# Kernel tuning notes

Measured on AMD Instinct MI355X. Metric: run time of the kernel, lower is better.

## Reference

```python
import jax, jax.numpy as jnp
import numpy as np

EPS = 1e-5  # torch LayerNorm default


def _ln(x, w, b):
    m = jnp.mean(x, axis=-1, keepdims=True)
    v = jnp.mean((x - m) ** 2, axis=-1, keepdims=True)
    return (x - m) / jnp.sqrt(v + EPS) * w + b


def _conv1x1(x, w, b):
    # x: [B,C,H,W], w: [O,C], b: [O]
    return jnp.einsum('bchw,oc->bohw', x, w) + b[None, :, None, None]


def setup_inputs() -> dict:
    key = jax.random.key(0)
    ks = jax.random.split(key, 5)
    B, Cin, H, W = 8, 384, 64, 64
    D, N = 128, 512
    s = lambda k, shape, scale=0.02: jax.random.normal(k, shape, jnp.float32) * scale
    return {
        'x': jax.random.normal(ks[0], (B, Cin, H, W), jnp.float32),
        'DR': jax.random.normal(ks[1], (N, D), jnp.float32),
        'conv_in_w': s(ks[2], (D, Cin)),
        'conv_in_b': jnp.zeros((D,), jnp.float32),
        'sem_w': s(ks[3], (D, D)),
        'sem_b': jnp.zeros((D,), jnp.float32),
        'norm1_w': jnp.ones((D,), jnp.float32),
        'norm1_b': jnp.zeros((D,), jnp.float32),
        'norm2_w': jnp.ones((D,), jnp.float32),
        'norm2_b': jnp.zeros((D,), jnp.float32),
        'conv_out_w': s(ks[4], (Cin, D)),
        'conv_out_b': jnp.zeros((Cin,), jnp.float32),
    }


def reference(x, DR, conv_in_w, conv_in_b, sem_w, sem_b, norm1_w, norm1_b,
              norm2_w, norm2_b, conv_out_w, conv_out_b):
    B, _, H, W = x.shape
    N = DR.shape[0]
    x_align = _conv1x1(x, conv_in_w, conv_in_b)                      # [B,D,H,W]
    x_sem = _conv1x1(x_align, sem_w, sem_b)                          # semantic_extra (1x1 conv)
    x_sem = x_sem.transpose(0, 2, 3, 1).reshape(B, H * W, -1)        # [B,HW,D]
    x_sem = _ln(x_sem, norm1_w, norm1_b)
    dr = _ln(DR, norm2_w, norm2_b).T                                 # [D,N] (same for all batches)
    # NOTE: original applies norm_1 TWICE for the numerator (faithful quirk)
    c_u = jnp.einsum('bld,dn->bln', _ln(x_sem, norm1_w, norm1_b), dr)  # [B,HW,N]
    c_d_l = jnp.sqrt(jnp.sum(x_sem ** 2, axis=-1, keepdims=True))      # [B,HW,1]
    c_d_r = jnp.sqrt(jnp.sum(dr ** 2, axis=0, keepdims=True))[None]    # [1,1,N]
    sim = c_u / (c_d_l * c_d_r)
    sim_soft = jax.nn.softmax(sim, axis=-1)                          # [B,HW,N]
    sim2d = sim_soft.transpose(0, 2, 1).reshape(B, N, H, W)
    degrad = jnp.einsum('bln,dn->bdl', sim_soft, dr).reshape(B, -1, H, W)  # [B,D,H,W]
    # pow-mask with per-batch min-max normalization
    mask_v = jnp.max(sim2d ** 3, axis=1, keepdims=True)              # [B,1,H,W]
    mn = jnp.min(mask_v.reshape(B, -1), axis=1).reshape(B, 1, 1, 1)
    mx = jnp.max(mask_v.reshape(B, -1), axis=1).reshape(B, 1, 1, 1)
    mask_v = 1.0 - (mask_v - mn) / (mx - mn)
    # topk row selection (torch fancy indexing gives [B,B,K,N]; squeeze(1) is a no-op for B>1)
    max_values = jnp.max(sim_soft, axis=2)                           # [B,HW]
    K = (H * W) // 50
    _, top_idx = jax.lax.top_k(max_values, K)                        # [B,K]
    results = jnp.take(sim_soft, top_idx, axis=1)                    # [B,B,K,N]
    out_img = _conv1x1(degrad, conv_out_w, conv_out_b)               # [B,Cin,H,W]
    return (mask_v, out_img, results)
```

## Files before the change

kernel.cpp:

```cpp
#include <hip/hip_runtime.h>
#include <cstdint>

#define EPS 1e-5f
#define BB   8
#define CIN  384
#define HWs  4096
#define LT   32768
#define DD   128
#define NN   512
#define TOPK 81
#define PSTR 528

typedef short short8 __attribute__((ext_vector_type(8)));
typedef float f32x4  __attribute__((ext_vector_type(4)));

__device__ __forceinline__ unsigned short f2bf(float x) {
  unsigned u = __float_as_uint(x);
  u += 0x7fffu + ((u >> 16) & 1u);
  return (unsigned short)(u >> 16);
}
__device__ __forceinline__ float bf2f(unsigned u16) {
  return __uint_as_float(u16 << 16);
}
__device__ __forceinline__ void put_frag(unsigned short* buf, int tile, int rc, int k, float v) {
  int ks = k >> 5, g = (k >> 3) & 3, j = k & 7;
  int basehw = ((tile * 4 + ks) * 2) * 512 + (g * 16 + rc) * 8 + j;
  unsigned short hi = f2bf(v);
  buf[basehw] = hi;
  buf[basehw + 512] = f2bf(v - bf2f(hi));
}

__global__ __launch_bounds__(64) void k_dr(const float* __restrict__ DR,
    const float* __restrict__ w2, const float* __restrict__ b2,
    const float* __restrict__ w1, const float* __restrict__ b1,
    unsigned short* __restrict__ drwF, unsigned short* __restrict__ drlnF,
    float* __restrict__ t2, float* __restrict__ rcr) {
  int n = blockIdx.x;
  int lane = threadIdx.x;
  const float* row = DR + n * DD;
  float x0 = row[lane], x1 = row[lane + 64];
  float s = x0 + x1, sq = x0 * x0 + x1 * x1;
  #pragma unroll
  for (int o = 32; o; o >>= 1) { s += __shfl_xor(s, o); sq += __shfl_xor(sq, o); }
  float m = s * (1.f / 128.f);
  float v = sq * (1.f / 128.f) - m * m;
  float inv = rsqrtf(v + EPS);
  float y0 = (x0 - m) * inv * w2[lane] + b2[lane];
  float y1 = (x1 - m) * inv * w2[lane + 64] + b2[lane + 64];
  int nt = n >> 4, cc = n & 15;
  put_frag(drwF, nt, cc, lane, y0 * w1[lane]);
  put_frag(drwF, nt, cc, lane + 64, y1 * w1[lane + 64]);
  int ks = n >> 5, gB = (n >> 3) & 3, j = n & 7;
  {
    int d = lane;
    unsigned short hi = f2bf(y0);
    int base = (((d >> 4) * 16 + ks) * 2) * 512 + (gB * 16 + (d & 15)) * 8 + j;
    drlnF[base] = hi;
    drlnF[base + 512] = f2bf(y0 - bf2f(hi));
  }
  {
    int d = lane + 64;
    unsigned short hi = f2bf(y1);
    int base = (((d >> 4) * 16 + ks) * 2) * 512 + (gB * 16 + (d & 15)) * 8 + j;
    drlnF[base] = hi;
    drlnF[base + 512] = f2bf(y1 - bf2f(hi));
  }
  float pt2 = y0 * b1[lane] + y1 * b1[lane + 64];
  float pss = y0 * y0 + y1 * y1;
  #pragma unroll
  for (int o = 32; o; o >>= 1) { pt2 += __shfl_xor(pt2, o); pss += __shfl_xor(pss, o); }
  if (lane == 0) { t2[n] = pt2; rcr[n] = rsqrtf(pss); }
}

__global__ __launch_bounds__(256) void k_bprep(const float* __restrict__ src,
                                               unsigned short* __restrict__ dst,
                                               int K) {
  int rt = blockIdx.x, kb = blockIdx.y;
  int t = threadIdx.x, m = t >> 4, kg = t & 15;
  int k0 = kb * 128 + kg * 8;
  const float* s = src + (size_t)(rt * 16 + m) * K + k0;
  float4 f0 = *(const float4*)s;
  float4 f1 = *(const float4*)(s + 4);
  float vs[8] = {f0.x, f0.y, f0.z, f0.w, f1.x, f1.y, f1.z, f1.w};
  short8 hi, lo;
  #pragma unroll
  for (int j = 0; j < 8; ++j) {
    unsigned short h = f2bf(vs[j]);
    hi[j] = (short)h;
    lo[j] = (short)f2bf(vs[j] - bf2f(h));
  }
  int nkt = K >> 5;
  int ks = k0 >> 5, g = (k0 >> 3) & 3;
  short8* D8 = (short8*)dst;
  int base = ((rt * nkt + ks) * 2) * 64 + g * 16 + m;
  D8[base] = hi;
  D8[base + 64] = lo;
}

__global__ __launch_bounds__(256, 3) void k_convsem(const float* __restrict__ x,
    const unsigned short* __restrict__ WinF, const float* __restrict__ bin,
    const unsigned short* __restrict__ semWF, const float* __restrict__ sb,
    const float* __restrict__ w1, const float* __restrict__ b1,
    unsigned short* __restrict__ ApF, float* __restrict__ rclv) {
  __shared__ float xt[CIN * 33];
  __shared__ float sredS[32][4], sredQ[32][4];
  __shared__ float rowM[32], rowI[32];
  int t = threadIdx.x;
  int w = t >> 6, lane = t & 63, m = lane & 15, g = lane >> 4;
  int l0 = blockIdx.x * 32;
  int b = l0 >> 12, hw0 = l0 & 4095;
  {
    const float* xs = x + (size_t)b * CIN * HWs + (size_t)(t >> 3) * HWs + hw0 + (t & 7) * 4;
    float4 v[12];
    #pragma unroll
    for (int r = 0; r < 12; ++r)
      v[r] = *(const float4*)(xs + (size_t)(r * 32) * HWs);
    #pragma unroll
    for (int r = 0; r < 12; ++r) {
      float* d = &xt[(r * 32 + (t >> 3)) * 33 + (t & 7) * 4];
      d[0] = v[r].x; d[1] = v[r].y; d[2] = v[r].z; d[3] = v[r].w;
    }
  }
  __syncthreads();
  const short8* B8 = (const short8*)WinF;
  f32x4 acc[2][2];
  #pragma unroll
  for (int lt = 0; lt < 2; ++lt)
    #pragma unroll
    for (int j2 = 0; j2 < 2; ++j2) acc[lt][j2] = (f32x4){0.f, 0.f, 0.f, 0.f};
  for (int ks = 0; ks < 12; ++ks) {
    short8 ah[2], al[2];
    #pragma unroll
    for (int lt = 0; lt < 2; ++lt) {
      #pragma unroll
      for (int j = 0; j < 8; ++j) {
        float xv = xt[(ks * 32 + g * 8 + j) * 33 + lt * 16 + m];
        unsigned short h = f2bf(xv);
        ah[lt][j] = (short)h;
        al[lt][j] = (short)f2bf(xv - bf2f(h));
      }
    }
    #pragma unroll
    for (int j2 = 0; j2 < 2; ++j2) {
      int dt = w * 2 + j2;
      short8 bh = B8[((dt * 12 + ks) * 2 + 0) * 64 + lane];
      short8 bl = B8[((dt * 12 + ks) * 2 + 1) * 64 + lane];
      #pragma unroll
      for (int lt = 0; lt < 2; ++lt) {
        acc[lt][j2] = __builtin_amdgcn_mfma_f32_16x16x32_bf16(ah[lt], bh, acc[lt][j2], 0, 0, 0);
        acc[lt][j2] = __builtin_amdgcn_mfma_f32_16x16x32_bf16(ah[lt], bl, acc[lt][j2], 0, 0, 0);
        acc[lt][j2] = __builtin_amdgcn_mfma_f32_16x16x32_bf16(al[lt], bh, acc[lt][j2], 0, 0, 0);
      }
    }
  }
  __syncthreads();
  unsigned int* plane = (unsigned int*)xt;
  {
    float bia[2] = {bin[w * 32 + m], bin[w * 32 + 16 + m]};
    #pragma unroll
    for (int lt = 0; lt < 2; ++lt)
      #pragma unroll
      for (int j2 = 0; j2 < 2; ++j2)
        #pragma unroll
        for (int r = 0; r < 4; ++r) {
          float v = acc[lt][j2][r] + bia[j2];
          unsigned short h = f2bf(v);
          unsigned short lo = f2bf(v - bf2f(h));
          plane[(lt * 16 + g * 4 + r) * 132 + (w * 2 + j2) * 16 + m] =
              (unsigned)h | ((unsigned)lo << 16);
        }
  }
  __syncthreads();
  const short8* S8 = (const short8*)semWF;
  f32x4 acc2[2][2];
  #pragma unroll
  for (int lt = 0; lt < 2; ++lt)
    #pragma unroll
    for (int j2 = 0; j2 < 2; ++j2) acc2[lt][j2] = (f32x4){0.f, 0.f, 0.f, 0.f};
  #pragma unroll
  for (int ks2 = 0; ks2 < 4; ++ks2) {
    short8 ah2[2], al2[2];
    #pragma unroll
    for (int lt = 0; lt < 2; ++lt) {
      const unsigned* src = &plane[(lt * 16 + m) * 132 + ks2 * 32 + g * 8];
      uint4 p0 = *(const uint4*)(src);
      uint4 p1 = *(const uint4*)(src + 4);
      unsigned uu[8] = {p0.x, p0.y, p0.z, p0.w, p1.x, p1.y, p1.z, p1.w};
      unsigned* ahp = (unsigned*)&ah2[lt];
      unsigned* alp = (unsigned*)&al2[lt];
      #pragma unroll
      for (int jj = 0; jj < 4; ++jj) {
        unsigned e0 = uu[2 * jj], e1 = uu[2 * jj + 1];
        ahp[jj] = (e0 & 0xffffu) | (e1 << 16);
        alp[jj] = (e0 >> 16) | (e1 & 0xffff0000u);
      }
    }
    #pragma unroll
    for (int j2 = 0; j2 < 2; ++j2) {
      int dt = w * 2 + j2;
      short8 bh = S8[((dt * 4 + ks2) * 2 + 0) * 64 + lane];
      short8 bl = S8[((dt * 4 + ks2) * 2 + 1) * 64 + lane];
      #pragma unroll
      for (int lt = 0; lt < 2; ++lt) {
        acc2[lt][j2] = __builtin_amdgcn_mfma_f32_16x16x32_bf16(ah2[lt], bh, acc2[lt][j2], 0, 0, 0);
        acc2[lt][j2] = __builtin_amdgcn_mfma_f32_16x16x32_bf16(ah2[lt], bl, acc2[lt][j2], 0, 0, 0);
        acc2[lt][j2] = __builtin_amdgcn_mfma_f32_16x16x32_bf16(al2[lt], bh, acc2[lt][j2], 0, 0, 0);
      }
    }
  }
  {
    float bia2[2] = {sb[w * 32 + m], sb[w * 32 + 16 + m]};
    #pragma unroll
    for (int lt = 0; lt < 2; ++lt)
      #pragma unroll
      for (int j2 = 0; j2 < 2; ++j2)
        #pragma unroll
        for (int r = 0; r < 4; ++r) acc2[lt][j2][r] += bia2[j2];
  }
  float s1[2][4], q1[2][4];
  #pragma unroll
  for (int lt = 0; lt < 2; ++lt)
    #pragma unroll
    for (int r = 0; r < 4; ++r) {
      float a = acc2[lt][0][r], b2v = acc2[lt][1][r];
      s1[lt][r] = a + b2v;
      q1[lt][r] = a * a + b2v * b2v;
    }
  #pragma unroll
  for (int o = 1; o < 16; o <<= 1)
    #pragma unroll
    for (int lt = 0; lt < 2; ++lt)
      #pragma unroll
      for (int r = 0; r < 4; ++r) {
        s1[lt][r] += __shfl_xor(s1[lt][r], o);
        q1[lt][r] += __shfl_xor(q1[lt][r], o);
      }
  if (m == 0) {
    #pragma unroll
    for (int lt = 0; lt < 2; ++lt)
      #pragma unroll
      for (int r = 0; r < 4; ++r) {
        sredS[lt * 16 + g * 4 + r][w] = s1[lt][r];
        sredQ[lt * 16 + g * 4 + r][w] = q1[lt][r];
      }
  }
  __syncthreads();
  if (t < 32) {
    float S = sredS[t][0] + sredS[t][1] + sredS[t][2] + sredS[t][3];
    float Q = sredQ[t][0] + sredQ[t][1] + sredQ[t][2] + sredQ[t][3];
    float mu = S * (1.f / 128.f);
    float var = Q * (1.f / 128.f) - mu * mu;
    rowM[t] = mu;
    rowI[t] = rsqrtf(var + EPS);
  }
  __syncthreads();
  float w1v[2] = {w1[w * 32 + m], w1[w * 32 + 16 + m]};
  float b1v[2] = {b1[w * 32 + m], b1[w * 32 + 16 + m]};
  #pragma unroll
  for (int lt = 0; lt < 2; ++lt)
    #pragma unroll
    for (int r = 0; r < 4; ++r) {
      float mu = rowM[lt * 16 + g * 4 + r];
      float iv = rowI[lt * 16 + g * 4 + r];
      float y0 = (acc2[lt][0][r] - mu) * iv * w1v[0] + b1v[0];
      float y1 = (acc2[lt][1][r] - mu) * iv * w1v[1] + b1v[1];
      acc2[lt][0][r] = y0; acc2[lt][1][r] = y1;
      s1[lt][r] = y0 + y1;
      q1[lt][r] = y0 * y0 + y1 * y1;
    }
  #pragma unroll
  for (int o = 1; o < 16; o <<= 1)
    #pragma unroll
    for (int lt = 0; lt < 2; ++lt)
      #pragma unroll
      for (int r = 0; r < 4; ++r) {
        s1[lt][r] += __shfl_xor(s1[lt][r], o);
        q1[lt][r] += __shfl_xor(q1[lt][r], o);
      }
  if (m == 0) {
    #pragma unroll
    for (int lt = 0; lt < 2; ++lt)
      #pragma unroll
      for (int r = 0; r < 4; ++r) {
        sredS[lt * 16 + g * 4 + r][w] = s1[lt][r];
        sredQ[lt * 16 + g * 4 + r][w] = q1[lt][r];
      }
  }
  __syncthreads();
  if (t < 32) {
    float S = sredS[t][0] + sredS[t][1] + sredS[t][2] + sredS[t][3];
    float Q = sredQ[t][0] + sredQ[t][1] + sredQ[t][2] + sredQ[t][3];
    float m2 = S * (1.f / 128.f);
    float v2 = Q * (1.f / 128.f) - m2 * m2;
    float inv2 = rsqrtf(v2 + EPS);
    float rcl = rsqrtf(Q);
    rowM[t] = m2;
    rowI[t] = inv2 * rcl;
    rclv[l0 + t] = rcl;
  }
  __syncthreads();
  float* planef = (float*)xt;
  #pragma unroll
  for (int lt = 0; lt < 2; ++lt)
    #pragma unroll
    for (int r = 0; r < 4; ++r) {
      float m2 = rowM[lt * 16 + g * 4 + r];
      float sc = rowI[lt * 16 + g * 4 + r];
      planef[(lt * 16 + g * 4 + r) * 132 + w * 32 + m] = (acc2[lt][0][r] - m2) * sc;
      planef[(lt * 16 + g * 4 + r) * 132 + w * 32 + 16 + m] = (acc2[lt][1][r] - m2) * sc;
    }
  __syncthreads();
  short8* O8 = (short8*)ApF;
  #pragma unroll
  for (int it = 0; it < 2; ++it) {
    int idx = it * 256 + t;
    int l = idx & 31, dq = idx >> 5;
    const float* src = &planef[l * 132 + dq * 8];
    float4 f0 = *(const float4*)src;
    float4 f1 = *(const float4*)(src + 4);
    float vs[8] = {f0.x, f0.y, f0.z, f0.w, f1.x, f1.y, f1.z, f1.w};
    short8 hi, lo;
    #pragma unroll
    for (int j = 0; j < 8; ++j) {
      unsigned short h = f2bf(vs[j]);
      hi[j] = (short)h;
      lo[j] = (short)f2bf(vs[j] - bf2f(h));
    }
    int ltg = (l0 + l) >> 4;
    int idx8 = ((ltg * 4 + (dq >> 2)) * 2) * 64 + (dq & 3) * 16 + (l & 15);
    O8[idx8] = hi;
    O8[idx8 + 64] = lo;
  }
}

__global__ __launch_bounds__(256, 4) void k_sdeg(const unsigned short* __restrict__ ApF,
    const unsigned short* __restrict__ drwF, const float* __restrict__ t2g,
    const float* __restrict__ rcrg, const float* __restrict__ rclg,
    const unsigned short* __restrict__ drlnF, const unsigned short* __restrict__ WoF,
    const float* __restrict__ bo,
    unsigned short* __restrict__ pF, float* __restrict__ maxv,
    float* __restrict__ out_img) {
  __shared__ __align__(16) float sredM[32][4];
  __shared__ __align__(16) float sredS[32][4];
  __shared__ __align__(16) unsigned short plds[32 * PSTR];
  int t = threadIdx.x;
  int w = t >> 6, lane = t & 63, c = lane & 15, g = lane >> 4;
  int l0 = blockIdx.x * 32;
  int lt0 = blockIdx.x * 2;
  const short8* A8 = (const short8*)ApF;
  const short8* B8 = (const short8*)drwF;
  f32x4 acc[2][8];
  #pragma unroll
  for (int il = 0; il < 2; ++il)
    #pragma unroll
    for (int jn = 0; jn < 8; ++jn) acc[il][jn] = (f32x4){0.f, 0.f, 0.f, 0.f};
  #pragma unroll
  for (int ks = 0; ks < 4; ++ks) {
    short8 ah0 = A8[((lt0 * 4 + ks) * 2 + 0) * 64 + lane];
    short8 al0 = A8[((lt0 * 4 + ks) * 2 + 1) * 64 + lane];
    short8 ah1 = A8[(((lt0 + 1) * 4 + ks) * 2 + 0) * 64 + lane];
    short8 al1 = A8[(((lt0 + 1) * 4 + ks) * 2 + 1) * 64 + lane];
    #pragma unroll
    for (int jn = 0; jn < 8; ++jn) {
      int nt = w * 8 + jn;
      short8 bh = B8[((nt * 4 + ks) * 2 + 0) * 64 + lane];
      short8 bl = B8[((nt * 4 + ks) * 2 + 1) * 64 + lane];
      acc[0][jn] = __builtin_amdgcn_mfma_f32_16x16x32_bf16(ah0, bh, acc[0][jn], 0, 0, 0);
      acc[0][jn] = __builtin_amdgcn_mfma_f32_16x16x32_bf16(ah0, bl, acc[0][jn], 0, 0, 0);
      acc[0][jn] = __builtin_amdgcn_mfma_f32_16x16x32_bf16(al0, bh, acc[0][jn], 0, 0, 0);
      acc[1][jn] = __builtin_amdgcn_mfma_f32_16x16x32_bf16(ah1, bh, acc[1][jn], 0, 0, 0);
      acc[1][jn] = __builtin_amdgcn_mfma_f32_16x16x32_bf16(ah1, bl, acc[1][jn], 0, 0, 0);
      acc[1][jn] = __builtin_amdgcn_mfma_f32_16x16x32_bf16(al1, bh, acc[1][jn], 0, 0, 0);
    }
  }
  float rcrv[8], t2v[8];
  #pragma unroll
  for (int jn = 0; jn < 8; ++jn) {
    int n = w * 128 + jn * 16 + c;
    rcrv[jn] = rcrg[n]; t2v[jn] = t2g[n];
  }
  float rclr[2][4];
  #pragma unroll
  for (int il = 0; il < 2; ++il)
    #pragma unroll
    for (int r = 0; r < 4; ++r)
      rclr[il][r] = rclg[l0 + il * 16 + g * 4 + r];
  float M[2][4];
  #pragma unroll
  for (int il = 0; il < 2; ++il)
    #pragma unroll
    for (int r = 0; r < 4; ++r) M[il][r] = -1e30f;
  #pragma unroll
  for (int il = 0; il < 2; ++il)
    #pragma unroll
    for (int jn = 0; jn < 8; ++jn) {
      f32x4 a = acc[il][jn];
      #pragma unroll
      for (int r = 0; r < 4; ++r) {
        float s = rcrv[jn] * (a[r] + rclr[il][r] * t2v[jn]);
        a[r] = s;
        M[il][r] = fmaxf(M[il][r], s);
      }
      acc[il][jn] = a;
    }
  #pragma unroll
  for (int o = 1; o < 16; o <<= 1)
    #pragma unroll
    for (int il = 0; il < 2; ++il)
      #pragma unroll
      for (int r = 0; r < 4; ++r)
        M[il][r] = fmaxf(M[il][r], __shfl_xor(M[il][r], o));
  if (c == 0) {
    #pragma unroll
    for (int il = 0; il < 2; ++il)
      #pragma unroll
      for (int r = 0; r < 4; ++r)
        sredM[il * 16 + g * 4 + r][w] = M[il][r];
  }
  __syncthreads();
  float Mf[2][4];
  #pragma unroll
  for (int il = 0; il < 2; ++il)
    #pragma unroll
    for (int r = 0; r < 4; ++r) {
      f32x4 mv = *(const f32x4*)(&sredM[il * 16 + g * 4 + r][0]);
      Mf[il][r] = fmaxf(fmaxf(mv[0], mv[1]), fmaxf(mv[2], mv[3]));
    }
  float S[2][4];
  #pragma unroll
  for (int il = 0; il < 2; ++il)
    #pragma unroll
    for (int r = 0; r < 4; ++r) S[il][r] = 0.f;
  #pragma unroll
  for (int il = 0; il < 2; ++il)
    #pragma unroll
    for (int jn = 0; jn < 8; ++jn) {
      f32x4 a = acc[il][jn];
      #pragma unroll
      for (int r = 0; r < 4; ++r) {
        float e = __expf(a[r] - Mf[il][r]);
        a[r] = e;
        S[il][r] += e;
      }
      acc[il][jn] = a;
    }
  #pragma unroll
  for (int o = 1; o < 16; o <<= 1)
    #pragma unroll
    for (int il = 0; il < 2; ++il)
      #pragma unroll
      for (int r = 0; r < 4; ++r)
        S[il][r] += __shfl_xor(S[il][r], o);
  if (c == 0) {
    #pragma unroll
    for (int il = 0; il < 2; ++il)
      #pragma unroll
      for (int r = 0; r < 4; ++r)
        sredS[il * 16 + g * 4 + r][w] = S[il][r];
  }
  __syncthreads();
  float RS[2][4];
  #pragma unroll
  for (int il = 0; il < 2; ++il)
    #pragma unroll
    for (int r = 0; r < 4; ++r) {
      f32x4 sv = *(const f32x4*)(&sredS[il * 16 + g * 4 + r][0]);
      float tot = sv[0] + sv[1] + sv[2] + sv[3];
      RS[il][r] = 1.f / tot;
    }
  if (w == 0 && c == 0) {
    #pragma unroll
    for (int il = 0; il < 2; ++il)
      #pragma unroll
      for (int r = 0; r < 4; ++r)
        maxv[l0 + il * 16 + g * 4 + r] = RS[il][r];
  }
  #pragma unroll
  for (int il = 0; il < 2; ++il)
    #pragma unroll
    for (int jn = 0; jn < 8; ++jn)
      #pragma unroll
      for (int r = 0; r < 4; ++r)
        plds[(il * 16 + g * 4 + r) * PSTR + w * 128 + jn * 16 + c] =
            f2bf(acc[il][jn][r] * RS[il][r]);
  __syncthreads();
  const short8* D8 = (const short8*)drlnF;
  f32x4 accd[2][2];
  #pragma unroll
  for (int lt = 0; lt < 2; ++lt)
    #pragma unroll
    for (int j2 = 0; j2 < 2; ++j2) accd[lt][j2] = (f32x4){0.f, 0.f, 0.f, 0.f};
  for (int ks = 0; ks < 16; ++ks) {
    const unsigned short* sp = &plds[c * PSTR + ks * 32 + g * 8];
    short8 pa0 = *(const short8*)sp;
    short8 pa1 = *(const short8*)(sp + 16 * PSTR);
    #pragma unroll
    for (int j2 = 0; j2 < 2; ++j2) {
      int dt = w * 2 + j2;
      short8 bh = D8[((dt * 16 + ks) * 2 + 0) * 64 + lane];
      short8 bl = D8[((dt * 16 + ks) * 2 + 1) * 64 + lane];
      accd[0][j2] = __builtin_amdgcn_mfma_f32_16x16x32_bf16(pa0, bh, accd[0][j2], 0, 0, 0);
      accd[0][j2] = __builtin_amdgcn_mfma_f32_16x16x32_bf16(pa0, bl, accd[0][j2], 0, 0, 0);
      accd[1][j2] = __builtin_amdgcn_mfma_f32_16x16x32_bf16(pa1, bh, accd[1][j2], 0, 0, 0);
      accd[1][j2] = __builtin_amdgcn_mfma_f32_16x16x32_bf16(pa1, bl, accd[1][j2], 0, 0, 0);
    }
  }
  short8* P8o = (short8*)pF;
  #pragma unroll
  for (int it = 0; it < 8; ++it) {
    int slot = it * 256 + t;
    int ltl = slot >> 10;
    int ks = (slot >> 6) & 15;
    int gB = (slot >> 4) & 3;
    int mrow = slot & 15;
    int row = ltl * 16 + mrow;
    int n0 = ks * 32 + gB * 8;
    short8 v = *(const short8*)(&plds[row * PSTR + n0]);
    P8o[blockIdx.x * 2048 + slot] = v;
  }
  __syncthreads();
  float* smem2 = (float*)plds;
  #pragma unroll
  for (int lt = 0; lt < 2; ++lt)
    #pragma unroll
    for (int j2 = 0; j2 < 2; ++j2)
      #pragma unroll
      for (int r = 0; r < 4; ++r)
        smem2[(lt * 16 + g * 4 + r) * 132 + w * 32 + j2 * 16 + c] = accd[lt][j2][r];
  __syncthreads();
  const short8* W8 = (const short8*)WoF;
  f32x4 acco[2][6];
  #pragma unroll
  for (int lt = 0; lt < 2; ++lt)
    #pragma unroll
    for (int ot = 0; ot < 6; ++ot) acco[lt][ot] = (f32x4){0.f, 0.f, 0.f, 0.f};
  #pragma unroll
  for (int ks2 = 0; ks2 < 4; ++ks2) {
    short8 dh[2];
    #pragma unroll
    for (int lt = 0; lt < 2; ++lt) {
      const float* src = &smem2[(lt * 16 + c) * 132 + ks2 * 32 + g * 8];
      float4 f0 = *(const float4*)src;
      float4 f1 = *(const float4*)(src + 4);
      float vs[8] = {f0.x, f0.y, f0.z, f0.w, f1.x, f1.y, f1.z, f1.w};
      #pragma unroll
      for (int j = 0; j < 8; ++j) dh[lt][j] = (short)f2bf(vs[j]);
    }
    #pragma unroll
    for (int ot = 0; ot < 6; ++ot) {
      int otg = w * 6 + ot;
      short8 wh = W8[((otg * 4 + ks2) * 2 + 0) * 64 + lane];
      short8 wl = W8[((otg * 4 + ks2) * 2 + 1) * 64 + lane];
      #pragma unroll
      for (int lt = 0; lt < 2; ++lt) {
        acco[lt][ot] = __builtin_amdgcn_mfma_f32_16x16x32_bf16(dh[lt], wh, acco[lt][ot], 0, 0, 0);
        acco[lt][ot] = __builtin_amdgcn_mfma_f32_16x16x32_bf16(dh[lt], wl, acco[lt][ot], 0, 0, 0);
      }
    }
  }
  int b = l0 >> 12, hw0 = l0 & 4095;
  float* ob = out_img + (size_t)b * CIN * HWs + hw0;
  #pragma unroll
  for (int ot = 0; ot < 6; ++ot) {
    float bov = bo[w * 96 + ot * 16 + c];
    #pragma unroll
    for (int lt = 0; lt < 2; ++lt) {
      f32x4 vv = acco[lt][ot];
      float4 o4 = {vv[0] + bov, vv[1] + bov, vv[2] + bov, vv[3] + bov};
      *(float4*)(ob + (size_t)(w * 96 + ot * 16 + c) * HWs + lt * 16 + g * 4) = o4;
    }
  }
}

__global__ __launch_bounds__(256) void k_topk(const float* __restrict__ maxv,
                                              int* __restrict__ tix,
                                              float* __restrict__ outm) {
  __shared__ unsigned int hist[4][256];
  __shared__ unsigned long long slist[TOPK];
  __shared__ unsigned long long bc_prefix;
  __shared__ int bc_need, scount;
  __shared__ float smn[4], smx[4];
  int b = blockIdx.x, t = threadIdx.x;
  int w = t >> 6;
  unsigned long long key[16];
  #pragma unroll
  for (int j = 0; j < 16; ++j) {
    int idx = t + j * 256;
    unsigned int bits = __float_as_uint(maxv[b * HWs + idx]);
    key[j] = ((unsigned long long)bits << 12) | (unsigned)(4095 - idx);
  }
  {
    float c3[16];
    float mn = 1e30f, mx = -1e30f;
    #pragma unroll
    for (int j = 0; j < 16; ++j) {
      float x = __uint_as_float((unsigned)(key[j] >> 12));
      float cc = x * x * x;
      c3[j] = cc;
      mn = fminf(mn, cc); mx = fmaxf(mx, cc);
    }
    #pragma unroll
    for (int o = 32; o; o >>= 1) { mn = fminf(mn, __shfl_xor(mn, o)); mx = fmaxf(mx, __shfl_xor(mx, o)); }
    if ((t & 63) == 0) { smn[w] = mn; smx[w] = mx; }
    __syncthreads();
    mn = fminf(fminf(smn[0], smn[1]), fminf(smn[2], smn[3]));
    mx = fmaxf(fmaxf(smx[0], smx[1]), fmaxf(smx[2], smx[3]));
    float sc = 1.f / (mx - mn);
    #pragma unroll
    for (int j = 0; j < 16; ++j)
      outm[b * HWs + t + j * 256] = 1.f - (c3[j] - mn) * sc;
  }
  if (t == 0) { bc_prefix = 0ull; bc_need = TOPK; scount = 0; }
  for (int r = 0; r < 6; ++r) {
    int shift = 40 - 8 * r;
    unsigned int* hflat = (unsigned int*)hist;
    hflat[t] = 0; hflat[t + 256] = 0; hflat[t + 512] = 0; hflat[t + 768] = 0;
    __syncthreads();
    unsigned long long prefix = bc_prefix;
    int bins[16];
    #pragma unroll
    for (int j = 0; j < 16; ++j)
      bins[j] = ((key[j] >> (shift + 8)) == prefix) ? (int)((key[j] >> shift) & 255) : -1;
    #pragma unroll
    for (int j = 0; j < 16; ++j) {
      if (bins[j] >= 0) {
        int cnt = 1;
        #pragma unroll
        for (int j2 = j + 1; j2 < 16; ++j2)
          if (bins[j2] == bins[j]) { bins[j2] = -1; ++cnt; }
        atomicAdd(&hist[w][bins[j]], (unsigned)cnt);
      }
    }
    __syncthreads();
    if (t < 64) {
      int cb[4], s = 0;
      #pragma unroll
      for (int j = 0; j < 4; ++j) {
        int bin = 255 - (t * 4 + j);
        cb[j] = (int)(hist[0][bin] + hist[1][bin] + hist[2][bin] + hist[3][bin]);
        s += cb[j];
      }
      int P = s;
      #pragma unroll
      for (int o = 1; o < 64; o <<= 1) {
        int u = __shfl_up(P, o);
        if (t >= o) P += u;
      }
      int need = bc_need;
      unsigned long long mask = __ballot(P >= need);
      int first = __ffsll((long long)mask) - 1;
      if (t == first) {
        int acc = P - s;
        #pragma unroll
        for (int j = 0; j < 4; ++j) {
          if (acc + cb[j] >= need) {
            bc_prefix = (prefix << 8) | (unsigned)(255 - (t * 4 + j));
            bc_need = need - acc;
            break;
          }
          acc += cb[j];
        }
      }
    }
    __syncthreads();
  }
  unsigned long long K81 = bc_prefix;
  #pragma unroll
  for (int j = 0; j < 16; ++j)
    if (key[j] >= K81) {
      int pos = atomicAdd(&scount, 1);
      slist[pos] = key[j];
    }
  __syncthreads();
  if (t < TOPK) {
    unsigned long long mine = slist[t];
    int rank = 0;
    for (int i = 0; i < TOPK; ++i) rank += (slist[i] > mine) ? 1 : 0;
    tix[b * TOPK + rank] = 4095 - (int)(mine & 0xFFFull);
  }
}

__global__ __launch_bounds__(128) void k_gather(const unsigned short* __restrict__ pF,
    const int* __restrict__ tix, float* __restrict__ outr) {
  int gB_ = blockIdx.x;
  int k = gB_ % TOPK;
  int bb = gB_ / TOPK;
  int b2 = bb & 7, b = bb >> 3;
  int l = b * HWs + tix[b2 * TOPK + k];
  int lt = l >> 4, mrow = l & 15;
  int t = threadIdx.x;
  int ks = t >> 3, gq = (t >> 1) & 3, j0 = (t & 1) * 4;
  int base = ((lt * 16 + ks) * 64 + gq * 16 + mrow) * 8 + j0;
  const unsigned* src = (const unsigned*)(pF + base);
  unsigned u0 = src[0], u1 = src[1];
  float4 v = {bf2f(u0 & 0xffffu), bf2f(u0 >> 16), bf2f(u1 & 0xffffu), bf2f(u1 >> 16)};
  *(float4*)(outr + (size_t)gB_ * NN + t * 4) = v;
}

extern "C" void kernel_launch(void* const* d_in, const int* in_sizes, int n_in,
                              void* d_out, int out_size, void* d_ws, size_t ws_size,
                              hipStream_t stream) {
  const float* x    = (const float*)d_in[0];
  const float* DR   = (const float*)d_in[1];
  const float* win  = (const float*)d_in[2];
  const float* bin  = (const float*)d_in[3];
  const float* sw   = (const float*)d_in[4];
  const float* sb   = (const float*)d_in[5];
  const float* n1w  = (const float*)d_in[6];
  const float* n1b  = (const float*)d_in[7];
  const float* n2w  = (const float*)d_in[8];
  const float* n2b  = (const float*)d_in[9];
  const float* wout = (const float*)d_in[10];
  const float* bout = (const float*)d_in[11];
  float* out = (float*)d_out;
  float* W = (float*)d_ws;

  unsigned short* drwF  = (unsigned short*)(W);
  float* t2   = W + 65536;
  float* rcr  = W + 66048;
  float* rclv = W + 66560;
  float* maxv = W + 99328;
  unsigned short* drlnF = (unsigned short*)(W + 132096);
  unsigned short* WoF   = (unsigned short*)(W + 197632);
  unsigned short* WinF  = (unsigned short*)(W + 246784);
  unsigned short* semWF = (unsigned short*)(W + 295936);
  unsigned short* ApF   = (unsigned short*)(W + 312320);
  unsigned short* pF    = (unsigned short*)(W + 4506624);
  int*   tix  = (int*)(W + 12895232);

  float* out_mask = out;
  float* out_img  = out + 32768;
  float* out_res  = out + 32768 + 12582912;

  k_dr     <<<NN, 64, 0, stream>>>(DR, n2w, n2b, n1w, n1b, drwF, drlnF, t2, rcr);
  k_bprep  <<<dim3(8, 3),  256, 0, stream>>>(win,  WinF,  CIN);
  k_bprep  <<<dim3(8, 1),  256, 0, stream>>>(sw,   semWF, DD);
  k_bprep  <<<dim3(24, 1), 256, 0, stream>>>(wout, WoF,   DD);
  k_convsem<<<1024, 256, 0, stream>>>(x, WinF, bin, semWF, sb, n1w, n1b, ApF, rclv);
  k_sdeg   <<<1024, 256, 0, stream>>>(ApF, drwF, t2, rcr, rclv, drlnF, WoF, bout,
                                      pF, maxv, out_img);
  k_topk   <<<BB,   256, 0, stream>>>(maxv, tix, out_mask);
  k_gather <<<BB * BB * TOPK, 128, 0, stream>>>(pF, tix, out_res);
}
```

Measured before the change: 217.5 us.

## Fuse conv/semantic kernel with similarity-softmax-degrad kernel via shared memory

Merges k_convsem and k_sdeg into a single k_mega kernel. The normalized activation fragments (ApF) and per-row reciprocal norms (rclv) now stay in LDS instead of going out to global memory and being read back, and one kernel launch is removed. LDS is unified into a single buffer reused across stages. In exchange, the fused kernel keeps the launch bound of 3 blocks per CU instead of 4 for the second stage, and its higher register and LDS pressure may lower occupancy.

```diff
diff --git a/kernel.cpp b/kernel.cpp
--- a/kernel.cpp
+++ b/kernel.cpp
@@ -97,18 +97,24 @@
   D8[base + 64] = lo;
 }
 
-__global__ __launch_bounds__(256, 3) void k_convsem(const float* __restrict__ x,
+__global__ __launch_bounds__(256, 3) void k_mega(const float* __restrict__ x,
     const unsigned short* __restrict__ WinF, const float* __restrict__ bin,
     const unsigned short* __restrict__ semWF, const float* __restrict__ sb,
     const float* __restrict__ w1, const float* __restrict__ b1,
-    unsigned short* __restrict__ ApF, float* __restrict__ rclv) {
-  __shared__ float xt[CIN * 33];
-  __shared__ float sredS[32][4], sredQ[32][4];
-  __shared__ float rowM[32], rowI[32];
+    const unsigned short* __restrict__ drwF, const float* __restrict__ t2g,
+    const float* __restrict__ rcrg,
+    const unsigned short* __restrict__ drlnF, const unsigned short* __restrict__ WoF,
+    const float* __restrict__ bo,
+    unsigned short* __restrict__ pF, float* __restrict__ maxv,
+    float* __restrict__ out_img) {
+  __shared__ __align__(16) float buf[12672];
+  __shared__ __align__(16) float sredS[32][4], sredQ[32][4];
+  __shared__ float rowM[32], rowI[32], rowRcl[32];
   int t = threadIdx.x;
   int w = t >> 6, lane = t & 63, m = lane & 15, g = lane >> 4;
   int l0 = blockIdx.x * 32;
   int b = l0 >> 12, hw0 = l0 & 4095;
+  float* xt = buf;
   {
     const float* xs = x + (size_t)b * CIN * HWs + (size_t)(t >> 3) * HWs + hw0 + (t & 7) * 4;
     float4 v[12];
@@ -154,7 +160,7 @@
     }
   }
   __syncthreads();
-  unsigned int* plane = (unsigned int*)xt;
+  unsigned int* plane = (unsigned int*)buf;
   {
     float bia[2] = {bin[w * 32 + m], bin[w * 32 + 16 + m]};
     #pragma unroll
@@ -296,10 +302,10 @@
     float rcl = rsqrtf(Q);
     rowM[t] = m2;
     rowI[t] = inv2 * rcl;
-    rclv[l0 + t] = rcl;
-  }
-  __syncthreads();
-  float* planef = (float*)xt;
+    rowRcl[t] = rcl;
+  }
+  __syncthreads();
+  float* planef = buf;
   #pragma unroll
   for (int lt = 0; lt < 2; ++lt)
     #pragma unroll
@@ -310,7 +316,7 @@
       planef[(lt * 16 + g * 4 + r) * 132 + w * 32 + 16 + m] = (acc2[lt][1][r] - m2) * sc;
     }
   __syncthreads();
-  short8* O8 = (short8*)ApF;
+  short8* ldsAp8 = (short8*)(buf + 8448);
   #pragma unroll
   for (int it = 0; it < 2; ++it) {
     int idx = it * 256 + t;
@@ -326,51 +332,36 @@
       hi[j] = (short)h;
       lo[j] = (short)f2bf(vs[j] - bf2f(h));
     }
-    int ltg = (l0 + l) >> 4;
-    int idx8 = ((ltg * 4 + (dq >> 2)) * 2) * 64 + (dq & 3) * 16 + (l & 15);
-    O8[idx8] = hi;
-    O8[idx8 + 64] = lo;
-  }
-}
-
-__global__ __launch_bounds__(256, 4) void k_sdeg(const unsigned short* __restrict__ ApF,
-    const unsigned short* __restrict__ drwF, const float* __restrict__ t2g,
-    const float* __restrict__ rcrg, const float* __restrict__ rclg,
-    const unsigned short* __restrict__ drlnF, const unsigned short* __restrict__ WoF,
-    const float* __restrict__ bo,
-    unsigned short* __restrict__ pF, float* __restrict__ maxv,
-    float* __restrict__ out_img) {
-  __shared__ __align__(16) float sredM[32][4];
-  __shared__ __align__(16) float sredS[32][4];
-  __shared__ __align__(16) unsigned short plds[32 * PSTR];
-  int t = threadIdx.x;
-  int w = t >> 6, lane = t & 63, c = lane & 15, g = lane >> 4;
-  int l0 = blockIdx.x * 32;
-  int lt0 = blockIdx.x * 2;
-  const short8* A8 = (const short8*)ApF;
-  const short8* B8 = (const short8*)drwF;
-  f32x4 acc[2][8];
-  #pragma unroll
-  for (int il = 0; il < 2; ++il)
-    #pragma unroll
-    for (int jn = 0; jn < 8; ++jn) acc[il][jn] = (f32x4){0.f, 0.f, 0.f, 0.f};
+    int ltl = l >> 4;
+    int idx8 = ((ltl * 4 + (dq >> 2)) * 2) * 64 + (dq & 3) * 16 + (l & 15);
+    ldsAp8[idx8] = hi;
+    ldsAp8[idx8 + 64] = lo;
+  }
+  __syncthreads();
+  int c = m;
+  const short8* B8s = (const short8*)drwF;
+  f32x4 accs[2][8];
+  #pragma unroll
+  for (int il = 0; il < 2; ++il)
+    #pragma unroll
+    for (int jn = 0; jn < 8; ++jn) accs[il][jn] = (f32x4){0.f, 0.f, 0.f, 0.f};
   #pragma unroll
   for (int ks = 0; ks < 4; ++ks) {
-    short8 ah0 = A8[((lt0 * 4 + ks) * 2 + 0) * 64 + lane];
-    short8 al0 = A8[((lt0 * 4 + ks) * 2 + 1) * 64 + lane];
-    short8 ah1 = A8[(((lt0 + 1) * 4 + ks) * 2 + 0) * 64 + lane];
-    short8 al1 = A8[(((lt0 + 1) * 4 + ks) * 2 + 1) * 64 + lane];
+    short8 ah0 = ldsAp8[((0 * 4 + ks) * 2 + 0) * 64 + lane];
+    short8 al0 = ldsAp8[((0 * 4 + ks) * 2 + 1) * 64 + lane];
+    short8 ah1 = ldsAp8[((1 * 4 + ks) * 2 + 0) * 64 + lane];
+    short8 al1 = ldsAp8[((1 * 4 + ks) * 2 + 1) * 64 + lane];
     #pragma unroll
     for (int jn = 0; jn < 8; ++jn) {
       int nt = w * 8 + jn;
-      short8 bh = B8[((nt * 4 + ks) * 2 + 0) * 64 + lane];
-      short8 bl = B8[((nt * 4 + ks) * 2 + 1) * 64 + lane];
-      acc[0][jn] = __builtin_amdgcn_mfma_f32_16x16x32_bf16(ah0, bh, acc[0][jn], 0, 0, 0);
-      acc[0][jn] = __builtin_amdgcn_mfma_f32_16x16x32_bf16(ah0, bl, acc[0][jn], 0, 0, 0);
-      acc[0][jn] = __builtin_amdgcn_mfma_f32_16x16x32_bf16(al0, bh, acc[0][jn], 0, 0, 0);
-      acc[1][jn] = __builtin_amdgcn_mfma_f32_16x16x32_bf16(ah1, bh, acc[1][jn], 0, 0, 0);
-      acc[1][jn] = __builtin_amdgcn_mfma_f32_16x16x32_bf16(ah1, bl, acc[1][jn], 0, 0, 0);
-      acc[1][jn] = __builtin_amdgcn_mfma_f32_16x16x32_bf16(al1, bh, acc[1][jn], 0, 0, 0);
+      short8 bh = B8s[((nt * 4 + ks) * 2 + 0) * 64 + lane];
+      short8 bl = B8s[((nt * 4 + ks) * 2 + 1) * 64 + lane];
+      accs[0][jn] = __builtin_amdgcn_mfma_f32_16x16x32_bf16(ah0, bh, accs[0][jn], 0, 0, 0);
+      accs[0][jn] = __builtin_amdgcn_mfma_f32_16x16x32_bf16(ah0, bl, accs[0][jn], 0, 0, 0);
+      accs[0][jn] = __builtin_amdgcn_mfma_f32_16x16x32_bf16(al0, bh, accs[0][jn], 0, 0, 0);
+      accs[1][jn] = __builtin_amdgcn_mfma_f32_16x16x32_bf16(ah1, bh, accs[1][jn], 0, 0, 0);
+      accs[1][jn] = __builtin_amdgcn_mfma_f32_16x16x32_bf16(ah1, bl, accs[1][jn], 0, 0, 0);
+      accs[1][jn] = __builtin_amdgcn_mfma_f32_16x16x32_bf16(al1, bh, accs[1][jn], 0, 0, 0);
     }
   }
   float rcrv[8], t2v[8];
@@ -384,7 +375,7 @@
   for (int il = 0; il < 2; ++il)
     #pragma unroll
     for (int r = 0; r < 4; ++r)
-      rclr[il][r] = rclg[l0 + il * 16 + g * 4 + r];
+      rclr[il][r] = rowRcl[il * 16 + g * 4 + r];
   float M[2][4];
   #pragma unroll
   for (int il = 0; il < 2; ++il)
@@ -394,14 +385,14 @@
   for (int il = 0; il < 2; ++il)
     #pragma unroll
     for (int jn = 0; jn < 8; ++jn) {
-      f32x4 a = acc[il][jn];
+      f32x4 a = accs[il][jn];
       #pragma unroll
       for (int r = 0; r < 4; ++r) {
         float s = rcrv[jn] * (a[r] + rclr[il][r] * t2v[jn]);
         a[r] = s;
         M[il][r] = fmaxf(M[il][r], s);
       }
-      acc[il][jn] = a;
+      accs[il][jn] = a;
     }
   #pragma unroll
   for (int o = 1; o < 16; o <<= 1)
@@ -415,7 +406,7 @@
     for (int il = 0; il < 2; ++il)
       #pragma unroll
       for (int r = 0; r < 4; ++r)
-        sredM[il * 16 + g * 4 + r][w] = M[il][r];
+        sredS[il * 16 + g * 4 + r][w] = M[il][r];
   }
   __syncthreads();
   float Mf[2][4];
@@ -423,7 +414,7 @@
   for (int il = 0; il < 2; ++il)
     #pragma unroll
     for (int r = 0; r < 4; ++r) {
-      f32x4 mv = *(const f32x4*)(&sredM[il * 16 + g * 4 + r][0]);
+      f32x4 mv = *(const f32x4*)(&sredS[il * 16 + g * 4 + r][0]);
       Mf[il][r] = fmaxf(fmaxf(mv[0], mv[1]), fmaxf(mv[2], mv[3]));
     }
   float S[2][4];
@@ -435,14 +426,14 @@
   for (int il = 0; il < 2; ++il)
     #pragma unroll
     for (int jn = 0; jn < 8; ++jn) {
-      f32x4 a = acc[il][jn];
+      f32x4 a = accs[il][jn];
       #pragma unroll
       for (int r = 0; r < 4; ++r) {
         float e = __expf(a[r] - Mf[il][r]);
         a[r] = e;
         S[il][r] += e;
       }
-      acc[il][jn] = a;
+      accs[il][jn] = a;
     }
   #pragma unroll
   for (int o = 1; o < 16; o <<= 1)
@@ -456,7 +447,7 @@
     for (int il = 0; il < 2; ++il)
       #pragma unroll
       for (int r = 0; r < 4; ++r)
-        sredS[il * 16 + g * 4 + r][w] = S[il][r];
+        sredQ[il * 16 + g * 4 + r][w] = S[il][r];
   }
   __syncthreads();
   float RS[2][4];
@@ -464,7 +455,7 @@
   for (int il = 0; il < 2; ++il)
     #pragma unroll
     for (int r = 0; r < 4; ++r) {
-      f32x4 sv = *(const f32x4*)(&sredS[il * 16 + g * 4 + r][0]);
+      f32x4 sv = *(const f32x4*)(&sredQ[il * 16 + g * 4 + r][0]);
       float tot = sv[0] + sv[1] + sv[2] + sv[3];
       RS[il][r] = 1.f / tot;
     }
@@ -475,6 +466,7 @@
       for (int r = 0; r < 4; ++r)
         maxv[l0 + il * 16 + g * 4 + r] = RS[il][r];
   }
+  unsigned short* plds = (unsigned short*)buf;
   #pragma unroll
   for (int il = 0; il < 2; ++il)
     #pragma unroll
@@ -482,7 +474,7 @@
       #pragma unroll
       for (int r = 0; r < 4; ++r)
         plds[(il * 16 + g * 4 + r) * PSTR + w * 128 + jn * 16 + c] =
-            f2bf(acc[il][jn][r] * RS[il][r]);
+            f2bf(accs[il][jn][r] * RS[il][r]);
   __syncthreads();
   const short8* D8 = (const short8*)drlnF;
   f32x4 accd[2][2];
@@ -519,7 +511,7 @@
     P8o[blockIdx.x * 2048 + slot] = v;
   }
   __syncthreads();
-  float* smem2 = (float*)plds;
+  float* smem2 = buf;
   #pragma unroll
   for (int lt = 0; lt < 2; ++lt)
     #pragma unroll
@@ -558,7 +550,6 @@
       }
     }
   }
-  int b = l0 >> 12, hw0 = l0 & 4095;
   float* ob = out_img + (size_t)b * CIN * HWs + hw0;
   #pragma unroll
   for (int ot = 0; ot < 6; ++ot) {
@@ -718,13 +709,11 @@
   unsigned short* drwF  = (unsigned short*)(W);
   float* t2   = W + 65536;
   float* rcr  = W + 66048;
-  float* rclv = W + 66560;
   float* maxv = W + 99328;
   unsigned short* drlnF = (unsigned short*)(W + 132096);
   unsigned short* WoF   = (unsigned short*)(W + 197632);
   unsigned short* WinF  = (unsigned short*)(W + 246784);
   unsigned short* semWF = (unsigned short*)(W + 295936);
-  unsigned short* ApF   = (unsigned short*)(W + 312320);
   unsigned short* pF    = (unsigned short*)(W + 4506624);
   int*   tix  = (int*)(W + 12895232);
 
@@ -736,8 +725,8 @@
   k_bprep  <<<dim3(8, 3),  256, 0, stream>>>(win,  WinF,  CIN);
   k_bprep  <<<dim3(8, 1),  256, 0, stream>>>(sw,   semWF, DD);
   k_bprep  <<<dim3(24, 1), 256, 0, stream>>>(wout, WoF,   DD);
-  k_convsem<<<1024, 256, 0, stream>>>(x, WinF, bin, semWF, sb, n1w, n1b, ApF, rclv);
-  k_sdeg   <<<1024, 256, 0, stream>>>(ApF, drwF, t2, rcr, rclv, drlnF, WoF, bout,
+  k_mega   <<<1024, 256, 0, stream>>>(x, WinF, bin, semWF, sb, n1w, n1b,
+                                      drwF, t2, rcr, drlnF, WoF, bout,
                                       pF, maxv, out_img);
   k_topk   <<<BB,   256, 0, stream>>>(maxv, tix, out_mask);
   k_gather <<<BB * BB * TOPK, 128, 0, stream>>>(pF, tix, out_res);
```

New measurement: 221.3 us. About the same (+1.7%).
